# Kernel tuning notes

Hardware: AMD Instinct MI355X
Metric: run time of the kernel (lower is better)

Reference implementation:

```python
import jax, jax.numpy as jnp
import numpy as np

NUM_HEADS = 8
LN_EPS = 1e-5

def setup_inputs() -> dict:
    key = jax.random.key(0)
    ks = jax.random.split(key, 8)
    B, C, H, W = 2, 512, 64, 64
    dim = C
    s = 1.0 / np.sqrt(dim)
    return {
        "pet_feat": jax.random.normal(ks[0], (B, C, H, W), jnp.float32),
        "ct_feat": jax.random.normal(ks[1], (B, C, H, W), jnp.float32),
        "Wq": jax.random.normal(ks[2], (dim, dim), jnp.float32) * s,
        "Wk": jax.random.normal(ks[3], (dim, dim), jnp.float32) * s,
        "Wv": jax.random.normal(ks[4], (dim, dim), jnp.float32) * s,
        "Wp": jax.random.normal(ks[5], (dim, dim), jnp.float32) * s,
        "bp": jnp.zeros((dim,), jnp.float32),
        "gamma": jnp.ones((dim,), jnp.float32),
        "beta": jnp.zeros((dim,), jnp.float32),
    }

def reference(pet_feat, ct_feat, Wq, Wk, Wv, Wp, bp, gamma, beta):
    B, C, H, W = pet_feat.shape
    L = H * W
    nh = NUM_HEADS
    hd = C // nh
    scale = hd ** (-0.5)
    # b c h w -> b (h w) c
    pet_seq = pet_feat.reshape(B, C, L).transpose(0, 2, 1)
    ct_seq = ct_feat.reshape(B, C, L).transpose(0, 2, 1)
    # linear projections (torch Linear: x @ W.T), split heads: b l (h d) -> b h l d
    q = (pet_seq @ Wq.T).reshape(B, L, nh, hd).transpose(0, 2, 1, 3)
    k = (ct_seq @ Wk.T).reshape(B, L, nh, hd).transpose(0, 2, 1, 3)
    v = (ct_seq @ Wv.T).reshape(B, L, nh, hd).transpose(0, 2, 1, 3)
    attn = jnp.einsum('bhld,bhmd->bhlm', q, k) * scale
    attn = jax.nn.softmax(attn, axis=-1)
    x = jnp.einsum('bhlm,bhmd->bhld', attn, v)
    # b h l d -> b l (h d)
    x = x.transpose(0, 2, 1, 3).reshape(B, L, C)
    x = x @ Wp.T + bp
    x = pet_seq + x
    # LayerNorm over channel dim
    mu = jnp.mean(x, axis=-1, keepdims=True)
    var = jnp.mean(jnp.square(x - mu), axis=-1, keepdims=True)
    x = (x - mu) * jax.lax.rsqrt(var + LN_EPS) * gamma + beta
    # b (h w) c -> b c h w
    return x.transpose(0, 2, 1).reshape(B, C, H, W)
```

## Files before the change

### kernel.cpp

```cpp
#include <hip/hip_runtime.h>

#define B_ 2
#define C_ 512
#define L_ 4096
#define NH 8
#define HD 64

typedef short bf16x8 __attribute__((ext_vector_type(8)));
typedef float f32x4 __attribute__((ext_vector_type(4)));
typedef unsigned short u16;
typedef unsigned short u16x8 __attribute__((ext_vector_type(8)));

static __device__ __forceinline__ u16 f2bf(float f) {
    union { float f; unsigned u; } v; v.f = f;
    unsigned u = v.u;
    u += 0x7fff + ((u >> 16) & 1);
    return (u16)(u >> 16);
}

static __device__ __forceinline__ unsigned cvtpk(float lo, float hi) {
    unsigned r;
    asm("v_cvt_pk_bf16_f32 %0, %1, %2" : "=v"(r) : "v"(lo), "v"(hi));
    return r;
}

__global__ __launch_bounds__(256) void transpose_conv_kernel(
        const float* __restrict__ src, u16* __restrict__ dst) {
    __shared__ float tile[64][65];
    int b  = blockIdx.z;
    int c0 = blockIdx.y * 64;
    int l0 = blockIdx.x * 64;
    int t  = threadIdx.x;
    int i  = t >> 2;
    int jc = (t & 3) * 16;
    const float* sp = src + ((size_t)(b * C_ + c0 + i)) * L_ + l0 + jc;
#pragma unroll
    for (int p = 0; p < 4; ++p) {
        float4 v = *(const float4*)(sp + p * 4);
        tile[i][jc + p * 4 + 0] = v.x;
        tile[i][jc + p * 4 + 1] = v.y;
        tile[i][jc + p * 4 + 2] = v.z;
        tile[i][jc + p * 4 + 3] = v.w;
    }
    __syncthreads();
    int cc = (t & 3) * 16;
    u16* dp = dst + ((size_t)(b * L_ + l0 + i)) * C_ + c0 + cc;
    u16x8 o0, o1;
#pragma unroll
    for (int q = 0; q < 8; ++q) o0[q] = f2bf(tile[cc + q][i]);
#pragma unroll
    for (int q = 0; q < 8; ++q) o1[q] = f2bf(tile[cc + 8 + q][i]);
    *(u16x8*)(dp)     = o0;
    *(u16x8*)(dp + 8) = o1;
}

__global__ __launch_bounds__(256) void f2bf4_kernel(
        const float* __restrict__ s0, const float* __restrict__ s1,
        const float* __restrict__ s2, const float* __restrict__ s3,
        u16* __restrict__ d0, u16* __restrict__ d1,
        u16* __restrict__ d2, u16* __restrict__ d3) {
    const int n = 512 * 512;
    int idx = blockIdx.x * blockDim.x + threadIdx.x;
    int stride = gridDim.x * blockDim.x;
    for (int i = idx; i < n; i += stride) {
        d0[i] = f2bf(s0[i]);
        d1[i] = f2bf(s1[i]);
        d2[i] = f2bf(s2[i]);
        d3[i] = f2bf(s3[i]);
    }
}

__global__ __launch_bounds__(256) void gemm_nt_kernel(
        const u16* __restrict__ A, const u16* __restrict__ Bt,
        u16* __restrict__ Cm, int M, int N, int K) {
    __shared__ u16 Al[64][72];
    __shared__ u16 Bl[64][72];
    int m0 = blockIdx.x * 64;
    int n0 = blockIdx.y * 64;
    int t = threadIdx.x;
    int w = t >> 6, lane = t & 63, ll = lane & 15, lh = lane >> 4;
    int moff = (w & 1) * 32, noff = (w >> 1) * 32;
    f32x4 acc[2][2] = {};
    int srow  = t >> 2;
    int skoff = (t & 3) * 16;
    const u16* Ap = A  + (size_t)(m0 + srow) * K + skoff;
    const u16* Bp = Bt + (size_t)(n0 + srow) * K + skoff;
    for (int kb = 0; kb < K; kb += 64) {
        u16x8 a0 = *(const u16x8*)(Ap + kb);
        u16x8 a1 = *(const u16x8*)(Ap + kb + 8);
        u16x8 b0 = *(const u16x8*)(Bp + kb);
        u16x8 b1 = *(const u16x8*)(Bp + kb + 8);
        *(u16x8*)&Al[srow][skoff]     = a0;
        *(u16x8*)&Al[srow][skoff + 8] = a1;
        *(u16x8*)&Bl[srow][skoff]     = b0;
        *(u16x8*)&Bl[srow][skoff + 8] = b1;
        __syncthreads();
#pragma unroll
        for (int kc = 0; kc < 2; ++kc) {
            bf16x8 af[2], bfr[2];
#pragma unroll
            for (int mf = 0; mf < 2; ++mf)
                af[mf] = *(const bf16x8*)&Al[moff + mf * 16 + ll][kc * 32 + lh * 8];
#pragma unroll
            for (int nf = 0; nf < 2; ++nf)
                bfr[nf] = *(const bf16x8*)&Bl[noff + nf * 16 + ll][kc * 32 + lh * 8];
#pragma unroll
            for (int mf = 0; mf < 2; ++mf)
#pragma unroll
                for (int nf = 0; nf < 2; ++nf)
                    acc[mf][nf] = __builtin_amdgcn_mfma_f32_16x16x32_bf16(
                        af[mf], bfr[nf], acc[mf][nf], 0, 0, 0);
        }
        __syncthreads();
    }
#pragma unroll
    for (int mf = 0; mf < 2; ++mf)
#pragma unroll
        for (int nf = 0; nf < 2; ++nf)
#pragma unroll
            for (int r = 0; r < 4; ++r) {
                int row = m0 + moff + mf * 16 + lh * 4 + r;
                int col = n0 + noff + nf * 16 + ll;
                Cm[(size_t)row * N + col] = f2bf(acc[mf][nf][r]);
            }
}

__global__ __launch_bounds__(256) void attn_kernel(
        const u16* __restrict__ q, const u16* __restrict__ k,
        const u16* __restrict__ vt, u16* __restrict__ X) {
    __shared__ u16 Kl[64][76];
    __shared__ u16 Vl[64][72];
    int l0 = blockIdx.x * 128;
    int h  = blockIdx.y;
    int b  = blockIdx.z;
    int t = threadIdx.x;
    int w = t >> 6, lane = t & 63, ll = lane & 15, lh = lane >> 4;
    const float C1 = 0.125f * 1.44269504088896340736f;
    const float M0 = 16.0f;

    bf16x8 qf[2][2];
#pragma unroll
    for (int u = 0; u < 2; ++u) {
        const u16* qp = q + ((size_t)(b * L_ + l0 + w * 32 + u * 16 + ll)) * C_
                          + h * HD + lh * 8;
        qf[u][0] = *(const bf16x8*)qp;
        qf[u][1] = *(const bf16x8*)(qp + 32);
    }
    int krow[4];
#pragma unroll
    for (int nf = 0; nf < 4; ++nf)
        krow[nf] = 32 * (nf & 1) + 4 * (nf >> 1) + 8 * (ll >> 2) + (ll & 3);

    int srow = t >> 2;
    int soff = (t & 3) * 16;
    const u16* kp = k  + ((size_t)(b * L_ + srow)) * C_ + h * HD + soff;
    const u16* vp = vt + ((size_t)(b * C_ + h * HD + srow)) * L_ + soff;

    f32x4 o[4][2] = {};
    float l_run[2] = {0.f, 0.f};

    for (int m0 = 0; m0 < L_; m0 += 64) {
        u16x8 ka0 = *(const u16x8*)(kp + (size_t)m0 * C_);
        u16x8 ka1 = *(const u16x8*)(kp + (size_t)m0 * C_ + 8);
        u16x8 va0 = *(const u16x8*)(vp + m0);
        u16x8 va1 = *(const u16x8*)(vp + m0 + 8);
        *(u16x8*)&Kl[srow][soff]     = ka0;
        *(u16x8*)&Kl[srow][soff + 8] = ka1;
        *(u16x8*)&Vl[srow][soff]     = va0;
        *(u16x8*)&Vl[srow][soff + 8] = va1;
        __syncthreads();

        bf16x8 kf[4][2], vf[4][2];
#pragma unroll
        for (int nf = 0; nf < 4; ++nf) {
            kf[nf][0] = *(const bf16x8*)&Kl[krow[nf]][lh * 8];
            kf[nf][1] = *(const bf16x8*)&Kl[krow[nf]][32 + lh * 8];
        }
#pragma unroll
        for (int df = 0; df < 4; ++df) {
            vf[df][0] = *(const bf16x8*)&Vl[df * 16 + ll][lh * 8];
            vf[df][1] = *(const bf16x8*)&Vl[df * 16 + ll][32 + lh * 8];
        }

        f32x4 s[2][4] = {};
#pragma unroll
        for (int kc = 0; kc < 2; ++kc)
#pragma unroll
            for (int nf = 0; nf < 4; ++nf)
#pragma unroll
                for (int u = 0; u < 2; ++u)
                    s[u][nf] = __builtin_amdgcn_mfma_f32_16x16x32_bf16(
                        kf[nf][kc], qf[u][kc], s[u][nf], 0, 0, 0);

        union { unsigned uu[4]; bf16x8 v; } pb[2][2];
#pragma unroll
        for (int u = 0; u < 2; ++u) {
            float ts = 0.f;
#pragma unroll
            for (int nf = 0; nf < 4; ++nf)
#pragma unroll
                for (int r = 0; r < 4; ++r) {
                    float pv = __builtin_amdgcn_exp2f(fmaf(s[u][nf][r], C1, -M0));
                    s[u][nf][r] = pv;
                    ts += pv;
                }
            l_run[u] += ts;
#pragma unroll
            for (int kc = 0; kc < 2; ++kc) {
                pb[kc][u].uu[0] = cvtpk(s[u][kc][0],     s[u][kc][1]);
                pb[kc][u].uu[1] = cvtpk(s[u][kc][2],     s[u][kc][3]);
                pb[kc][u].uu[2] = cvtpk(s[u][kc + 2][0], s[u][kc + 2][1]);
                pb[kc][u].uu[3] = cvtpk(s[u][kc + 2][2], s[u][kc + 2][3]);
            }
        }
#pragma unroll
        for (int kc = 0; kc < 2; ++kc)
#pragma unroll
            for (int df = 0; df < 4; ++df)
#pragma unroll
                for (int u = 0; u < 2; ++u)
                    o[df][u] = __builtin_amdgcn_mfma_f32_16x16x32_bf16(
                        vf[df][kc], pb[kc][u].v, o[df][u], 0, 0, 0);
        __syncthreads();
    }

#pragma unroll
    for (int u = 0; u < 2; ++u) {
        l_run[u] += __shfl_xor(l_run[u], 16, 64);
        l_run[u] += __shfl_xor(l_run[u], 32, 64);
    }
#pragma unroll
    for (int u = 0; u < 2; ++u) {
        float inv = 1.f / l_run[u];
        u16* xp = X + ((size_t)(b * L_ + l0 + w * 32 + u * 16 + ll)) * C_
                    + h * HD + 4 * lh;
#pragma unroll
        for (int df = 0; df < 4; ++df) {
            union { unsigned uu[2]; } pk;
            pk.uu[0] = cvtpk(o[df][u][0] * inv, o[df][u][1] * inv);
            pk.uu[1] = cvtpk(o[df][u][2] * inv, o[df][u][3] * inv);
            *(uint2*)(xp + df * 16) = *(uint2*)pk.uu;
        }
    }
}

__global__ __launch_bounds__(256) void outln_kernel(
        const u16* __restrict__ X, const u16* __restrict__ Wpb,
        const float* __restrict__ bp, const float* __restrict__ gamma,
        const float* __restrict__ beta, const float* __restrict__ pet,
        float* __restrict__ out) {
    __shared__ u16 Al[16][520];
    __shared__ float red[16][4][2];
    int g0 = blockIdx.x * 16;
    int b  = g0 >> 12;
    int l0 = g0 & (L_ - 1);
    int t = threadIdx.x;
    int w = t >> 6, lane = t & 63, ll = lane & 15, lh = lane >> 4;
    {
        int row  = t >> 4;
        int koff = (t & 15) * 32;
        const u16* xp = X + ((size_t)(g0 + row)) * C_ + koff;
#pragma unroll
        for (int p = 0; p < 4; ++p)
            *(u16x8*)&Al[row][koff + p * 8] = *(const u16x8*)(xp + p * 8);
    }
    __syncthreads();
    int nbase = w * 128;
    f32x4 acc[8] = {};
    for (int kc = 0; kc < 16; ++kc) {
        bf16x8 af = *(const bf16x8*)&Al[ll][kc * 32 + lh * 8];
#pragma unroll
        for (int nf = 0; nf < 8; ++nf) {
            int c = nbase + nf * 16 + ll;
            bf16x8 bfr = *(const bf16x8*)(Wpb + (size_t)c * C_ + kc * 32 + lh * 8);
            acc[nf] = __builtin_amdgcn_mfma_f32_16x16x32_bf16(af, bfr, acc[nf], 0, 0, 0);
        }
    }
    float psum[4] = {}, psq[4] = {};
#pragma unroll
    for (int nf = 0; nf < 8; ++nf) {
        int c = nbase + nf * 16 + ll;
        float bias = bp[c];
#pragma unroll
        for (int r = 0; r < 4; ++r) {
            int l = l0 + lh * 4 + r;
            float v = acc[nf][r] + bias + pet[((size_t)(b * C_ + c)) * L_ + l];
            acc[nf][r] = v;
            psum[r] += v;
            psq[r]  += v * v;
        }
    }
#pragma unroll
    for (int x = 1; x < 16; x <<= 1)
#pragma unroll
        for (int r = 0; r < 4; ++r) {
            psum[r] += __shfl_xor(psum[r], x, 64);
            psq[r]  += __shfl_xor(psq[r], x, 64);
        }
    if (ll == 0) {
#pragma unroll
        for (int r = 0; r < 4; ++r) {
            red[lh * 4 + r][w][0] = psum[r];
            red[lh * 4 + r][w][1] = psq[r];
        }
    }
    __syncthreads();
#pragma unroll
    for (int r = 0; r < 4; ++r) {
        int row = lh * 4 + r;
        float s  = red[row][0][0] + red[row][1][0] + red[row][2][0] + red[row][3][0];
        float sq = red[row][0][1] + red[row][1][1] + red[row][2][1] + red[row][3][1];
        float mean = s * (1.f / 512.f);
        float var  = sq * (1.f / 512.f) - mean * mean;
        float rs = rsqrtf(var + 1e-5f);
        int l = l0 + row;
#pragma unroll
        for (int nf = 0; nf < 8; ++nf) {
            int c = nbase + nf * 16 + ll;
            float v = (acc[nf][r] - mean) * rs * gamma[c] + beta[c];
            out[((size_t)(b * C_ + c)) * L_ + l] = v;
        }
    }
}

extern "C" void kernel_launch(void* const* d_in, const int* in_sizes, int n_in,
                              void* d_out, int out_size, void* d_ws, size_t ws_size,
                              hipStream_t stream) {
    const float* pet   = (const float*)d_in[0];
    const float* ct    = (const float*)d_in[1];
    const float* Wq    = (const float*)d_in[2];
    const float* Wk    = (const float*)d_in[3];
    const float* Wv    = (const float*)d_in[4];
    const float* Wp    = (const float*)d_in[5];
    const float* bp    = (const float*)d_in[6];
    const float* gamma = (const float*)d_in[7];
    const float* beta  = (const float*)d_in[8];
    float* out = (float*)d_out;

    char* ws = (char*)d_ws;
    const size_t SZ = (size_t)B_ * L_ * C_ * 2;
    u16* petT = (u16*)(ws);
    u16* ctT  = (u16*)(ws + SZ);
    u16* qb   = (u16*)(ws + 2 * SZ);
    u16* kb   = (u16*)(ws + 3 * SZ);
    u16* vtb  = (u16*)(ws + 4 * SZ);
    u16* wqb  = (u16*)(ws + 5 * SZ);
    u16* wkb  = wqb + 512 * 512;
    u16* wvb  = wkb + 512 * 512;
    u16* wpb  = wvb + 512 * 512;

    dim3 tb(256);
    transpose_conv_kernel<<<dim3(L_ / 64, C_ / 64, B_), tb, 0, stream>>>(pet, petT);
    transpose_conv_kernel<<<dim3(L_ / 64, C_ / 64, B_), tb, 0, stream>>>(ct, ctT);
    f2bf4_kernel<<<dim3(256), tb, 0, stream>>>(Wq, Wk, Wv, Wp, wqb, wkb, wvb, wpb);

    gemm_nt_kernel<<<dim3((B_ * L_) / 64, C_ / 64), tb, 0, stream>>>(
        petT, wqb, qb, B_ * L_, C_, C_);
    gemm_nt_kernel<<<dim3((B_ * L_) / 64, C_ / 64), tb, 0, stream>>>(
        ctT, wkb, kb, B_ * L_, C_, C_);
    gemm_nt_kernel<<<dim3(C_ / 64, L_ / 64), tb, 0, stream>>>(
        wvb, ctT, vtb, C_, L_, C_);
    gemm_nt_kernel<<<dim3(C_ / 64, L_ / 64), tb, 0, stream>>>(
        wvb, ctT + (size_t)L_ * C_, vtb + (size_t)C_ * L_, C_, L_, C_);

    u16* Xb = petT;
    attn_kernel<<<dim3(L_ / 128, NH, B_), tb, 0, stream>>>(qb, kb, vtb, Xb);

    outln_kernel<<<dim3((B_ * L_) / 16), tb, 0, stream>>>(
        Xb, wpb, bp, gamma, beta, pet, out);
}
```

Measured before the change: 197.5 us.

## Double-buffer K/V tiles in attention and merge the two transpose launches

The attention kernel now keeps two LDS buffers for K and V. Each iteration issues the global loads for the next tile before computing on the current one, and stores them into the other buffer afterwards, so one barrier per iteration remains instead of two. This aims to hide global-load latency behind the MFMA work, at the cost of doubled LDS use, which may lower occupancy. The two input transpose/convert launches are also combined into one grid with twice the z extent, saving one kernel launch.

```diff
diff --git a/kernel.cpp b/kernel.cpp
--- a/kernel.cpp
+++ b/kernel.cpp
@@ -25,9 +25,13 @@
 }
 
 __global__ __launch_bounds__(256) void transpose_conv_kernel(
-        const float* __restrict__ src, u16* __restrict__ dst) {
+        const float* __restrict__ pet, const float* __restrict__ ct,
+        u16* __restrict__ petT, u16* __restrict__ ctT) {
     __shared__ float tile[64][65];
-    int b  = blockIdx.z;
+    int z  = blockIdx.z;
+    int b  = z >> 1;
+    const float* src = (z & 1) ? ct : pet;
+    u16* dst         = (z & 1) ? ctT : petT;
     int c0 = blockIdx.y * 64;
     int l0 = blockIdx.x * 64;
     int t  = threadIdx.x;
@@ -128,8 +132,8 @@
 __global__ __launch_bounds__(256) void attn_kernel(
         const u16* __restrict__ q, const u16* __restrict__ k,
         const u16* __restrict__ vt, u16* __restrict__ X) {
-    __shared__ u16 Kl[64][76];
-    __shared__ u16 Vl[64][72];
+    __shared__ u16 Kl[2][64][76];
+    __shared__ u16 Vl[2][64][72];
     int l0 = blockIdx.x * 128;
     int h  = blockIdx.y;
     int b  = blockIdx.z;
@@ -156,30 +160,43 @@
     const u16* kp = k  + ((size_t)(b * L_ + srow)) * C_ + h * HD + soff;
     const u16* vp = vt + ((size_t)(b * C_ + h * HD + srow)) * L_ + soff;
 
+    u16x8 ka0 = *(const u16x8*)(kp);
+    u16x8 ka1 = *(const u16x8*)(kp + 8);
+    u16x8 va0 = *(const u16x8*)(vp);
+    u16x8 va1 = *(const u16x8*)(vp + 8);
+    *(u16x8*)&Kl[0][srow][soff]     = ka0;
+    *(u16x8*)&Kl[0][srow][soff + 8] = ka1;
+    *(u16x8*)&Vl[0][srow][soff]     = va0;
+    *(u16x8*)&Vl[0][srow][soff + 8] = va1;
+    kp += (size_t)64 * C_;
+    vp += 64;
+
     f32x4 o[4][2] = {};
     float l_run[2] = {0.f, 0.f};
 
-    for (int m0 = 0; m0 < L_; m0 += 64) {
-        u16x8 ka0 = *(const u16x8*)(kp + (size_t)m0 * C_);
-        u16x8 ka1 = *(const u16x8*)(kp + (size_t)m0 * C_ + 8);
-        u16x8 va0 = *(const u16x8*)(vp + m0);
-        u16x8 va1 = *(const u16x8*)(vp + m0 + 8);
-        *(u16x8*)&Kl[srow][soff]     = ka0;
-        *(u16x8*)&Kl[srow][soff + 8] = ka1;
-        *(u16x8*)&Vl[srow][soff]     = va0;
-        *(u16x8*)&Vl[srow][soff + 8] = va1;
+    int cur = 0;
+    const int NT = L_ / 64;
+    for (int tile = 0; tile < NT; ++tile) {
         __syncthreads();
-
+        const bool pre = (tile < NT - 1);
+        if (pre) {
+            ka0 = *(const u16x8*)(kp);
+            ka1 = *(const u16x8*)(kp + 8);
+            va0 = *(const u16x8*)(vp);
+            va1 = *(const u16x8*)(vp + 8);
+            kp += (size_t)64 * C_;
+            vp += 64;
+        }
         bf16x8 kf[4][2], vf[4][2];
 #pragma unroll
         for (int nf = 0; nf < 4; ++nf) {
-            kf[nf][0] = *(const bf16x8*)&Kl[krow[nf]][lh * 8];
-            kf[nf][1] = *(const bf16x8*)&Kl[krow[nf]][32 + lh * 8];
+            kf[nf][0] = *(const bf16x8*)&Kl[cur][krow[nf]][lh * 8];
+            kf[nf][1] = *(const bf16x8*)&Kl[cur][krow[nf]][32 + lh * 8];
         }
 #pragma unroll
         for (int df = 0; df < 4; ++df) {
-            vf[df][0] = *(const bf16x8*)&Vl[df * 16 + ll][lh * 8];
-            vf[df][1] = *(const bf16x8*)&Vl[df * 16 + ll][32 + lh * 8];
+            vf[df][0] = *(const bf16x8*)&Vl[cur][df * 16 + ll][lh * 8];
+            vf[df][1] = *(const bf16x8*)&Vl[cur][df * 16 + ll][32 + lh * 8];
         }
 
         f32x4 s[2][4] = {};
@@ -221,7 +238,15 @@
                 for (int u = 0; u < 2; ++u)
                     o[df][u] = __builtin_amdgcn_mfma_f32_16x16x32_bf16(
                         vf[df][kc], pb[kc][u].v, o[df][u], 0, 0, 0);
-        __syncthreads();
+
+        if (pre) {
+            int nxt = cur ^ 1;
+            *(u16x8*)&Kl[nxt][srow][soff]     = ka0;
+            *(u16x8*)&Kl[nxt][srow][soff + 8] = ka1;
+            *(u16x8*)&Vl[nxt][srow][soff]     = va0;
+            *(u16x8*)&Vl[nxt][srow][soff + 8] = va1;
+            cur = nxt;
+        }
     }
 
 #pragma unroll
@@ -350,8 +375,8 @@
     u16* wpb  = wvb + 512 * 512;
 
     dim3 tb(256);
-    transpose_conv_kernel<<<dim3(L_ / 64, C_ / 64, B_), tb, 0, stream>>>(pet, petT);
-    transpose_conv_kernel<<<dim3(L_ / 64, C_ / 64, B_), tb, 0, stream>>>(ct, ctT);
+    transpose_conv_kernel<<<dim3(L_ / 64, C_ / 64, 2 * B_), tb, 0, stream>>>(
+        pet, ct, petT, ctT);
     f2bf4_kernel<<<dim3(256), tb, 0, stream>>>(Wq, Wk, Wv, Wp, wqb, wkb, wvb, wpb);
 
     gemm_nt_kernel<<<dim3((B_ * L_) / 64, C_ / 64), tb, 0, stream>>>(
```

After: 186.7 us. 1.06x faster.
